# Kernel tuning notes

Measured on AMD Instinct MI355X. Metric: run time of the kernel, lower is better.

## Reference

```python
import jax, jax.numpy as jnp
import numpy as np

KD = 3  # kernel size per spatial dim
K = KD * KD * KD  # 27 taps


def conv3d(x, w, b, padding=1):
    # x: [B, C, D, H, W], w: [O, C, kd, kh, kw]
    pad = ((padding, padding),) * 3
    y = jax.lax.conv_general_dilated(
        x, w, window_strides=(1, 1, 1), padding=pad,
        dimension_numbers=('NCDHW', 'OIDHW', 'NCDHW'))
    return y + b[None, :, None, None, None]


def add_coords(x):
    # CoordConv: append 3 normalized coordinate channels in [-1, 1].
    B, C, D, H, W = x.shape
    z = jnp.linspace(-1.0, 1.0, D, dtype=x.dtype)[:, None, None]
    y = jnp.linspace(-1.0, 1.0, H, dtype=x.dtype)[None, :, None]
    xx = jnp.linspace(-1.0, 1.0, W, dtype=x.dtype)[None, None, :]
    coords = jnp.stack([
        jnp.broadcast_to(z, (D, H, W)),
        jnp.broadcast_to(y, (D, H, W)),
        jnp.broadcast_to(xx, (D, H, W)),
    ], axis=0)  # [3, D, H, W]
    coords = jnp.broadcast_to(coords[None], (B, 3, D, H, W))
    return jnp.concatenate([x, coords], axis=1)


def trilinear_sample(x, pos):
    # x: [B, C, D, H, W]; pos: [B, K, 3, D, H, W] absolute (z, y, x) sample coords.
    # Zero padding outside the volume. Returns [B, C, K, D, H, W].
    B, C, D, H, W = x.shape
    Kt = pos.shape[1]
    pz, py, px = pos[:, :, 0], pos[:, :, 1], pos[:, :, 2]  # [B, K, D, H, W]
    fz, fy, fx = jnp.floor(pz), jnp.floor(py), jnp.floor(px)
    x_flat = x.reshape(B, C, D * H * W)
    out = jnp.zeros((B, C, Kt, D, H, W), dtype=x.dtype)
    for cz in (0.0, 1.0):
        for cy in (0.0, 1.0):
            for cx in (0.0, 1.0):
                iz, iy, ix = fz + cz, fy + cy, fx + cx
                wgt = ((1.0 - jnp.abs(pz - iz)) *
                       (1.0 - jnp.abs(py - iy)) *
                       (1.0 - jnp.abs(px - ix)))
                valid = ((iz >= 0) & (iz < D) & (iy >= 0) & (iy < H)
                         & (ix >= 0) & (ix < W))
                izc = jnp.clip(iz, 0, D - 1).astype(jnp.int32)
                iyc = jnp.clip(iy, 0, H - 1).astype(jnp.int32)
                ixc = jnp.clip(ix, 0, W - 1).astype(jnp.int32)
                flat = ((izc * H + iyc) * W + ixc).reshape(B, -1)  # [B, K*DHW]
                vals = jax.vmap(lambda xf, idx: jnp.take(xf, idx, axis=1))(x_flat, flat)
                vals = vals.reshape(B, C, Kt, D, H, W)
                out = out + (wgt * valid.astype(x.dtype))[:, None] * vals
    return out


def modulated_deform_conv3d(x, offsets, alpha, w, b):
    # x: [B, Cin, D, H, W]; offsets: [B, 3K, D, H, W]; alpha: [B, K, D, H, W]
    # w: [O, Cin, 3, 3, 3]; stride 1, padding 1, dilation 1.
    B, Cin, D, H, W = x.shape
    off = offsets.reshape(B, K, 3, D, H, W)
    # Base sampling grid per tap: voxel position + kernel offset (pad=1 -> -1..1).
    dz = jnp.arange(D, dtype=x.dtype)[:, None, None]
    dy = jnp.arange(H, dtype=x.dtype)[None, :, None]
    dx = jnp.arange(W, dtype=x.dtype)[None, None, :]
    base = jnp.stack([
        jnp.broadcast_to(dz, (D, H, W)),
        jnp.broadcast_to(dy, (D, H, W)),
        jnp.broadcast_to(dx, (D, H, W)),
    ], axis=0)  # [3, D, H, W]
    kg = jnp.arange(KD, dtype=x.dtype) - 1.0  # [-1, 0, 1]
    kpos = jnp.stack(jnp.meshgrid(kg, kg, kg, indexing='ij'),
                     axis=-1).reshape(K, 3)  # [K, 3] in (kd, kh, kw) order
    pos = base[None, None] + kpos[None, :, :, None, None, None] + off  # [B,K,3,D,H,W]
    sampled = trilinear_sample(x, pos)  # [B, Cin, K, D, H, W]
    sampled = sampled * alpha[:, None]  # modulation
    wk = w.reshape(w.shape[0], Cin, K)
    out = jnp.einsum('bckv,ock->bov', sampled.reshape(B, Cin, K, D * H * W), wk)
    return out.reshape(B, -1, D, H, W) + b[None, :, None, None, None]


def setup_inputs() -> dict:
    key = jax.random.key(0)
    ks = jax.random.split(key, 4)
    B, Cin, Cout, D, H, W = 2, 64, 64, 8, 32, 32
    x = jax.random.normal(ks[0], (B, Cin, D, H, W), dtype=jnp.float32)
    # Small init on offset branch keeps sampling near the regular grid.
    w_off = jax.random.normal(ks[1], (108, Cin + 3, 3, 3, 3), jnp.float32) * 0.01
    b_off = jnp.zeros((108,), jnp.float32)
    w_dcn = jax.random.normal(ks[2], (Cout, Cin, 3, 3, 3), jnp.float32) * (1.0 / np.sqrt(Cin * 27))
    b_dcn = jnp.zeros((Cout,), jnp.float32)
    return {"x": x, "w_off": w_off, "b_off": b_off, "w_dcn": w_dcn, "b_dcn": b_dcn}


def reference(x, w_off, b_off, w_dcn, b_dcn):
    # CoordConv3d offset/mask prediction
    pred = conv3d(add_coords(x), w_off, b_off, padding=1)  # [B, 108, D, H, W]
    offsets, alpha = pred[:, :81], pred[:, 81:]
    alpha = jax.nn.sigmoid(alpha)  # [B, 27, D, H, W]
    return modulated_deform_conv3d(x, offsets, alpha, w_dcn, b_dcn)
```

## Files before the change

kernel.cpp:

```cpp
#include <hip/hip_runtime.h>

#define DHW  8192
#define COFF 108

typedef __attribute__((ext_vector_type(8))) short bf16x8;
typedef __attribute__((ext_vector_type(4))) float f32x4;
typedef __bf16 bfv2 __attribute__((ext_vector_type(2)));

__device__ inline unsigned short f2bf(float f) {
    unsigned u = __float_as_uint(f);
    u += 0x7fffu + ((u >> 16) & 1u);
    return (unsigned short)(u >> 16);
}
__device__ inline float bf2f(unsigned short h) {
    return __uint_as_float(((unsigned)h) << 16);
}

__device__ inline float dot2bf(unsigned a, unsigned b, float c) {
#if defined(__has_builtin) && __has_builtin(__builtin_amdgcn_fdot2_f32_bf16)
    return __builtin_amdgcn_fdot2_f32_bf16(__builtin_bit_cast(bfv2, a),
                                           __builtin_bit_cast(bfv2, b), c, false);
#else
    c += __uint_as_float(a << 16) * __uint_as_float(b << 16);
    c += __uint_as_float(a & 0xffff0000u) * __uint_as_float(b & 0xffff0000u);
    return c;
#endif
}

__global__ __launch_bounds__(256) void k_prep(
    const float* __restrict__ x, const float* __restrict__ w_off,
    const float* __restrict__ w_dcn,
    ushort* __restrict__ xt, ushort* __restrict__ pA1,
    ushort* __restrict__ pAc, ushort* __restrict__ pW)
{
    __shared__ ushort tile[16 * 66];
    const int bi = blockIdx.x;
    const int tid = threadIdx.x;
    if (bi < 1024) {
        const int b  = bi >> 9;
        const int f0 = (bi & 511) * 16;
        #pragma unroll
        for (int it = 0; it < 4; ++it) {
            int c = it * 16 + (tid >> 4), f = tid & 15;
            tile[f * 66 + c] = f2bf(x[((size_t)(b * 64 + c)) * DHW + f0 + f]);
        }
        __syncthreads();
        #pragma unroll
        for (int it = 0; it < 4; ++it) {
            int f = it * 4 + (tid >> 6), c = tid & 63;
            xt[((size_t)b * DHW + f0 + f) * 64 + c] = tile[f * 66 + c];
        }
    } else {
        int t0 = (bi - 1024) * 256 + tid;
        const int stride = 32 * 256;
        for (int i = t0; i < 27 * 2 * 7 * 512; i += stride) {
            int j = i & 7, l = (i >> 3) & 63, rest = i >> 9;
            int m = rest % 7, ch = (rest / 7) & 1, tap = rest / 14;
            int co = m * 16 + (l & 15);
            int ci = ch * 32 + (l >> 4) * 8 + j;
            pA1[i] = (co < COFF) ? f2bf(w_off[(co * 67 + ci) * 27 + tap]) : (ushort)0;
        }
        for (int i = t0; i < 3 * 7 * 512; i += stride) {
            int j = i & 7, l = (i >> 3) & 63, rest = i >> 9;
            int m = rest % 7, t = rest / 7;
            int co = m * 16 + (l & 15);
            int flatk = t * 32 + (l >> 4) * 8 + j;
            ushort v = 0;
            if (co < COFF && flatk < 81) {
                int cc = flatk / 27, tap = flatk % 27;
                v = f2bf(w_off[(co * 67 + 64 + cc) * 27 + tap]);
            }
            pAc[i] = v;
        }
        for (int i = t0; i < 27 * 2 * 4 * 512; i += stride) {
            int j = i & 7, l = (i >> 3) & 63;
            int m = (i >> 9) & 3, ch = (i >> 11) & 1, k = i >> 12;
            int o = m * 16 + (l & 15);
            int c = ch * 32 + (l >> 4) * 8 + j;
            pW[i] = f2bf(w_dcn[(o * 64 + c) * 27 + k]);
        }
    }
}

__global__ __launch_bounds__(512, 4) void k_fused(
    const ushort* __restrict__ xt, const ushort* __restrict__ pA1,
    const ushort* __restrict__ pAc, const ushort* __restrict__ pW,
    const float* __restrict__ b_off, const float* __restrict__ b_dcn,
    float* __restrict__ out)
{
    __shared__ __align__(16) char smem[64256];
    ushort* pred_lds = (ushort*)smem;
    char*   region   = smem + 6912;

    const int bi   = blockIdx.x;
    const int b    = bi >> 8;
    const int sp32 = bi & 255;
    const int d    = sp32 >> 5;
    const int h    = sp32 & 31;
    const int spg  = sp32 * 32;
    const int tid  = threadIdx.x;
    const int wv = tid >> 6, lane = tid & 63, q = lane >> 4, r16 = lane & 15;
    const ushort* __restrict__ xb = xt + (size_t)b * DHW * 64;

    f32x4 acc1[14] = {};
    for (int c = wv; c < 57; c += 8) {
        bf16x8 bf[2];
        const ushort* pa;
        if (c < 54) {
            int tap = c >> 1, ch = c & 1;
            int dz = tap / 9, rem9 = tap - dz * 9, dy = rem9 / 3, dx = rem9 - dy * 3;
            int zz = d + dz - 1, yy = h + dy - 1;
            int basepos = (zz << 10) + (yy << 5);
            bool okzy = ((unsigned)zz < 8u) & ((unsigned)yy < 32u);
            #pragma unroll
            for (int pt = 0; pt < 2; ++pt) {
                int xx = pt * 16 + r16 + dx - 1;
                bool ok = okzy & ((unsigned)xx < 32u);
                bf16x8 tv = {};
                if (ok) tv = *(const bf16x8*)(xb + (size_t)(basepos + xx) * 64
                                              + ch * 32 + q * 8);
                bf[pt] = tv;
            }
            pa = pA1 + (size_t)((tap * 2 + ch) * 7) * 512 + lane * 8;
        } else {
            int t = c - 54;
            #pragma unroll
            for (int pt = 0; pt < 2; ++pt) {
                bf16x8 bt;
                #pragma unroll
                for (int j = 0; j < 8; ++j) {
                    int flatk = t * 32 + q * 8 + j;
                    int cc = flatk / 27, tap = flatk % 27;
                    int dz = tap / 9, rem9 = tap - dz * 9, dy = rem9 / 3, dx = rem9 - dy * 3;
                    int zz = d + dz - 1, yy = h + dy - 1, xx = pt * 16 + r16 + dx - 1;
                    bool ok = (flatk < 81) & ((unsigned)zz < 8u) & ((unsigned)yy < 32u)
                              & ((unsigned)xx < 32u);
                    float val = 0.f;
                    if (ok)
                        val = (cc == 0) ? (-1.f + (2.f / 7.f) * (float)zz)
                            : (cc == 1) ? (-1.f + (2.f / 31.f) * (float)yy)
                                        : (-1.f + (2.f / 31.f) * (float)xx);
                    bt[j] = (short)f2bf(val);
                }
                bf[pt] = bt;
            }
            pa = pAc + (size_t)(t * 7) * 512 + lane * 8;
        }
        #pragma unroll
        for (int m = 0; m < 7; ++m) {
            bf16x8 af = *(const bf16x8*)(pa + m * 512);
            acc1[m * 2 + 0] = __builtin_amdgcn_mfma_f32_16x16x32_bf16(af, bf[0], acc1[m * 2 + 0], 0, 0, 0);
            acc1[m * 2 + 1] = __builtin_amdgcn_mfma_f32_16x16x32_bf16(af, bf[1], acc1[m * 2 + 1], 0, 0, 0);
        }
    }
    {
        uint2* red1 = (uint2*)region;
        #pragma unroll
        for (int i = 0; i < 14; ++i) {
            f32x4 s = acc1[i];
            uint2 pk2;
            pk2.x = (unsigned)f2bf(s[0]) | ((unsigned)f2bf(s[1]) << 16);
            pk2.y = (unsigned)f2bf(s[2]) | ((unsigned)f2bf(s[3]) << 16);
            red1[(wv * 14 + i) * 64 + lane] = pk2;
        }
        __syncthreads();
        for (int i = wv; i < 14; i += 8) {
            float s0 = 0.f, s1 = 0.f, s2 = 0.f, s3 = 0.f;
            #pragma unroll
            for (int sw = 0; sw < 8; ++sw) {
                uint2 v = red1[(sw * 14 + i) * 64 + lane];
                s0 += bf2f((unsigned short)(v.x & 0xffffu));
                s1 += bf2f((unsigned short)(v.x >> 16));
                s2 += bf2f((unsigned short)(v.y & 0xffffu));
                s3 += bf2f((unsigned short)(v.y >> 16));
            }
            int m = i >> 1, pt = i & 1;
            float sr[4] = {s0, s1, s2, s3};
            #pragma unroll
            for (int r = 0; r < 4; ++r) {
                int co = m * 16 + q * 4 + r;
                if (co < COFF)
                    pred_lds[co * 32 + pt * 16 + r16] = f2bf(sr[r] + b_off[co]);
            }
        }
        __syncthreads();
    }

    uint4* cwi = (uint4*)region;
    uint4* cww = (uint4*)(region + 27648);
    for (int kp = tid; kp < 27 * 32; kp += 512) {
        int k = kp >> 5, p = kp & 31;
        float offz = bf2f(pred_lds[(k * 3 + 0) * 32 + p]);
        float offy = bf2f(pred_lds[(k * 3 + 1) * 32 + p]);
        float offx = bf2f(pred_lds[(k * 3 + 2) * 32 + p]);
        float av   = bf2f(pred_lds[(81 + k) * 32 + p]);
        float alpha = 1.f / (1.f + __expf(-av));
        int kz = k / 9, rem = k - kz * 9, ky = rem / 3, kx = rem - ky * 3;
        float pz = (float)(d + kz - 1) + offz;
        float py = (float)(h + ky - 1) + offy;
        float px = (float)(p + kx - 1) + offx;
        float fz = floorf(pz), fy = floorf(py), fx = floorf(px);
        float tz = pz - fz, ty = py - fy, tx = px - fx;
        int iz0 = (int)fz, iy0 = (int)fy, ix0 = (int)fx;
        unsigned idxs[8]; float wgts[8];
        #pragma unroll
        for (int c8 = 0; c8 < 8; ++c8) {
            int czi = c8 >> 2, cyi = (c8 >> 1) & 1, cxi = c8 & 1;
            int iz = iz0 + czi, iy = iy0 + cyi, ix = ix0 + cxi;
            float wz = czi ? tz : 1.f - tz;
            float wy = cyi ? ty : 1.f - ty;
            float wx = cxi ? tx : 1.f - tx;
            bool ok = ((unsigned)iz < 8u) && ((unsigned)iy < 32u) && ((unsigned)ix < 32u);
            idxs[c8] = ok ? ((unsigned)((iz << 10) + (iy << 5) + ix) << 7) : 0u;
            wgts[c8] = ok ? wz * wy * wx * alpha : 0.f;
        }
        cwi[(k * 2 + 0) * 32 + p] = make_uint4(idxs[0], idxs[1], idxs[2], idxs[3]);
        cwi[(k * 2 + 1) * 32 + p] = make_uint4(idxs[4], idxs[5], idxs[6], idxs[7]);
        cww[k * 32 + p] = make_uint4(
            (unsigned)f2bf(wgts[0]) | ((unsigned)f2bf(wgts[1]) << 16),
            (unsigned)f2bf(wgts[2]) | ((unsigned)f2bf(wgts[3]) << 16),
            (unsigned)f2bf(wgts[4]) | ((unsigned)f2bf(wgts[5]) << 16),
            (unsigned)f2bf(wgts[6]) | ((unsigned)f2bf(wgts[7]) << 16));
    }
    __syncthreads();

    const int pt2 = wv & 1, ch2 = (wv >> 1) & 1, kh = wv >> 2;
    const int pr = lane >> 2, cg = lane & 3;
    const int p2 = pt2 * 16 + pr;
    const char* xbB = (const char*)xb + ch2 * 64 + cg * 16;
    const int baddr = (r16 * 4 + q) << 2;
    f32x4 acc2[4] = {};
    for (int k = kh; k < 27; k += 2) {
        uint4 wq = cww[k * 32 + p2];
        uint4 i0 = cwi[(k * 2 + 0) * 32 + p2];
        uint4 i1 = cwi[(k * 2 + 1) * 32 + p2];
        unsigned iv[8] = {i0.x, i0.y, i0.z, i0.w, i1.x, i1.y, i1.z, i1.w};
        uint4 xv[8];
        #pragma unroll
        for (int c8 = 0; c8 < 8; ++c8)
            xv[c8] = *(const uint4*)(xbB + iv[c8]);
        unsigned wp[4] = {wq.x, wq.y, wq.z, wq.w};
        float sa[8] = {};
        #pragma unroll
        for (int cp = 0; cp < 4; ++cp) {
            unsigned ua[4] = {xv[cp * 2 + 0].x, xv[cp * 2 + 0].y, xv[cp * 2 + 0].z, xv[cp * 2 + 0].w};
            unsigned ub[4] = {xv[cp * 2 + 1].x, xv[cp * 2 + 1].y, xv[cp * 2 + 1].z, xv[cp * 2 + 1].w};
            #pragma unroll
            for (int dw = 0; dw < 4; ++dw) {
                unsigned plo = __builtin_amdgcn_perm(ub[dw], ua[dw], 0x05040100u);
                unsigned phi = __builtin_amdgcn_perm(ub[dw], ua[dw], 0x07060302u);
                sa[dw * 2 + 0] = dot2bf(plo, wp[cp], sa[dw * 2 + 0]);
                sa[dw * 2 + 1] = dot2bf(phi, wp[cp], sa[dw * 2 + 1]);
            }
        }
        unsigned pk0 = (unsigned)f2bf(sa[0]) | ((unsigned)f2bf(sa[1]) << 16);
        unsigned pk1 = (unsigned)f2bf(sa[2]) | ((unsigned)f2bf(sa[3]) << 16);
        unsigned pk2 = (unsigned)f2bf(sa[4]) | ((unsigned)f2bf(sa[5]) << 16);
        unsigned pk3 = (unsigned)f2bf(sa[6]) | ((unsigned)f2bf(sa[7]) << 16);
        uint4 bd;
        bd.x = (unsigned)__builtin_amdgcn_ds_bpermute(baddr, (int)pk0);
        bd.y = (unsigned)__builtin_amdgcn_ds_bpermute(baddr, (int)pk1);
        bd.z = (unsigned)__builtin_amdgcn_ds_bpermute(baddr, (int)pk2);
        bd.w = (unsigned)__builtin_amdgcn_ds_bpermute(baddr, (int)pk3);
        bf16x8 bfrag = __builtin_bit_cast(bf16x8, bd);
        const ushort* pwk = pW + (size_t)((k * 2 + ch2) * 4) * 512 + lane * 8;
        #pragma unroll
        for (int m = 0; m < 4; ++m)
            acc2[m] = __builtin_amdgcn_mfma_f32_16x16x32_bf16(
                *(const bf16x8*)(pwk + m * 512), bfrag, acc2[m], 0, 0, 0);
    }

    __syncthreads();
    f32x4* red2 = (f32x4*)region;
    #pragma unroll
    for (int m = 0; m < 4; ++m)
        red2[(wv * 4 + m) * 64 + lane] = acc2[m];
    __syncthreads();
    {
        const int mo = wv >> 1, pto = wv & 1;
        f32x4 s = red2[((pto + 0) * 4 + mo) * 64 + lane]
                + red2[((pto + 2) * 4 + mo) * 64 + lane]
                + red2[((pto + 4) * 4 + mo) * 64 + lane]
                + red2[((pto + 6) * 4 + mo) * 64 + lane];
        float* __restrict__ outb = out + (size_t)b * 64 * DHW + spg;
        #pragma unroll
        for (int r = 0; r < 4; ++r) {
            int o = mo * 16 + q * 4 + r;
            outb[(size_t)o * DHW + pto * 16 + r16] = s[r] + b_dcn[o];
        }
    }
}

extern "C" void kernel_launch(void* const* d_in, const int* in_sizes, int n_in,
                              void* d_out, int out_size, void* d_ws, size_t ws_size,
                              hipStream_t stream) {
    const float* x     = (const float*)d_in[0];
    const float* w_off = (const float*)d_in[1];
    const float* b_off = (const float*)d_in[2];
    const float* w_dcn = (const float*)d_in[3];
    const float* b_dcn = (const float*)d_in[4];
    float* out = (float*)d_out;

    ushort* xt  = (ushort*)d_ws;
    ushort* pA1 = (ushort*)((char*)d_ws + 2097152);
    ushort* pAc = (ushort*)((char*)d_ws + 2484224);
    ushort* pW  = (ushort*)((char*)d_ws + 2505728);

    k_prep <<<1056, 256, 0, stream>>>(x, w_off, w_dcn, xt, pA1, pAc, pW);
    k_fused<<<512, 512, 0, stream>>>(xt, pA1, pAc, pW, b_off, b_dcn, out);
}
```

Before: 64.42 us.

## Split fused kernel into offset-conv and deform-conv kernels with double-buffered gathers

The single fused kernel is split in two. The first computes the offset/mask convolution and writes the prediction to a global workspace buffer in bf16. The second reads that buffer, builds the sampling indices and weights, and runs the deformable gather+MFMA loop with software double-buffering, so the gathers for tap k+2 are issued before the compute for tap k. The goal is to give each kernel lower LDS and register pressure and to hide gather latency, at the cost of an extra launch and a global round trip for the predictions.

Measured after the change: 68.60 us. 6.5% more time.

```diff
diff --git a/kernel.cpp b/kernel.cpp
--- a/kernel.cpp
+++ b/kernel.cpp
@@ -82,15 +82,12 @@
     }
 }
 
-__global__ __launch_bounds__(512, 4) void k_fused(
+__global__ __launch_bounds__(512, 4) void k_conv(
     const ushort* __restrict__ xt, const ushort* __restrict__ pA1,
-    const ushort* __restrict__ pAc, const ushort* __restrict__ pW,
-    const float* __restrict__ b_off, const float* __restrict__ b_dcn,
-    float* __restrict__ out)
+    const ushort* __restrict__ pAc, const float* __restrict__ b_off,
+    ushort* __restrict__ predg)
 {
-    __shared__ __align__(16) char smem[64256];
-    ushort* pred_lds = (ushort*)smem;
-    char*   region   = smem + 6912;
+    __shared__ __align__(16) char smem[57344];
 
     const int bi   = blockIdx.x;
     const int b    = bi >> 8;
@@ -153,47 +150,110 @@
             acc1[m * 2 + 1] = __builtin_amdgcn_mfma_f32_16x16x32_bf16(af, bf[1], acc1[m * 2 + 1], 0, 0, 0);
         }
     }
-    {
-        uint2* red1 = (uint2*)region;
-        #pragma unroll
-        for (int i = 0; i < 14; ++i) {
-            f32x4 s = acc1[i];
-            uint2 pk2;
-            pk2.x = (unsigned)f2bf(s[0]) | ((unsigned)f2bf(s[1]) << 16);
-            pk2.y = (unsigned)f2bf(s[2]) | ((unsigned)f2bf(s[3]) << 16);
-            red1[(wv * 14 + i) * 64 + lane] = pk2;
-        }
-        __syncthreads();
-        for (int i = wv; i < 14; i += 8) {
-            float s0 = 0.f, s1 = 0.f, s2 = 0.f, s3 = 0.f;
-            #pragma unroll
-            for (int sw = 0; sw < 8; ++sw) {
-                uint2 v = red1[(sw * 14 + i) * 64 + lane];
-                s0 += bf2f((unsigned short)(v.x & 0xffffu));
-                s1 += bf2f((unsigned short)(v.x >> 16));
-                s2 += bf2f((unsigned short)(v.y & 0xffffu));
-                s3 += bf2f((unsigned short)(v.y >> 16));
-            }
-            int m = i >> 1, pt = i & 1;
-            float sr[4] = {s0, s1, s2, s3};
-            #pragma unroll
-            for (int r = 0; r < 4; ++r) {
-                int co = m * 16 + q * 4 + r;
-                if (co < COFF)
-                    pred_lds[co * 32 + pt * 16 + r16] = f2bf(sr[r] + b_off[co]);
-            }
-        }
-        __syncthreads();
-    }
-
-    uint4* cwi = (uint4*)region;
-    uint4* cww = (uint4*)(region + 27648);
+    uint2* red1 = (uint2*)smem;
+    #pragma unroll
+    for (int i = 0; i < 14; ++i) {
+        f32x4 s = acc1[i];
+        uint2 pk2;
+        pk2.x = (unsigned)f2bf(s[0]) | ((unsigned)f2bf(s[1]) << 16);
+        pk2.y = (unsigned)f2bf(s[2]) | ((unsigned)f2bf(s[3]) << 16);
+        red1[(wv * 14 + i) * 64 + lane] = pk2;
+    }
+    __syncthreads();
+    ushort* __restrict__ predb = predg + (size_t)b * COFF * DHW + spg;
+    for (int i = wv; i < 14; i += 8) {
+        float s0 = 0.f, s1 = 0.f, s2 = 0.f, s3 = 0.f;
+        #pragma unroll
+        for (int sw = 0; sw < 8; ++sw) {
+            uint2 v = red1[(sw * 14 + i) * 64 + lane];
+            s0 += bf2f((unsigned short)(v.x & 0xffffu));
+            s1 += bf2f((unsigned short)(v.x >> 16));
+            s2 += bf2f((unsigned short)(v.y & 0xffffu));
+            s3 += bf2f((unsigned short)(v.y >> 16));
+        }
+        int m = i >> 1, pt = i & 1;
+        float sr[4] = {s0, s1, s2, s3};
+        #pragma unroll
+        for (int r = 0; r < 4; ++r) {
+            int co = m * 16 + q * 4 + r;
+            if (co < COFF)
+                predb[(size_t)co * DHW + pt * 16 + r16] = f2bf(sr[r] + b_off[co]);
+        }
+    }
+}
+
+#define LOADCW(X, kk) do {                                                    \
+    uint4 wq_ = cww[(kk) * 32 + p2];                                          \
+    uint4 i0_ = cwi[((kk) * 2 + 0) * 32 + p2];                                \
+    uint4 i1_ = cwi[((kk) * 2 + 1) * 32 + p2];                                \
+    wp##X[0] = wq_.x; wp##X[1] = wq_.y; wp##X[2] = wq_.z; wp##X[3] = wq_.w;   \
+    xv##X[0] = *(const uint4*)(xbB + i0_.x);                                  \
+    xv##X[1] = *(const uint4*)(xbB + i0_.y);                                  \
+    xv##X[2] = *(const uint4*)(xbB + i0_.z);                                  \
+    xv##X[3] = *(const uint4*)(xbB + i0_.w);                                  \
+    xv##X[4] = *(const uint4*)(xbB + i1_.x);                                  \
+    xv##X[5] = *(const uint4*)(xbB + i1_.y);                                  \
+    xv##X[6] = *(const uint4*)(xbB + i1_.z);                                  \
+    xv##X[7] = *(const uint4*)(xbB + i1_.w);                                  \
+} while (0)
+
+#define COMPUTE(X, kk) do {                                                   \
+    float sa[8] = {0.f, 0.f, 0.f, 0.f, 0.f, 0.f, 0.f, 0.f};                   \
+    _Pragma("unroll")                                                         \
+    for (int cp = 0; cp < 4; ++cp) {                                          \
+        unsigned ua[4] = {xv##X[cp*2].x, xv##X[cp*2].y, xv##X[cp*2].z, xv##X[cp*2].w};       \
+        unsigned ub[4] = {xv##X[cp*2+1].x, xv##X[cp*2+1].y, xv##X[cp*2+1].z, xv##X[cp*2+1].w};\
+        _Pragma("unroll")                                                     \
+        for (int dw = 0; dw < 4; ++dw) {                                      \
+            unsigned plo = __builtin_amdgcn_perm(ub[dw], ua[dw], 0x05040100u);\
+            unsigned phi = __builtin_amdgcn_perm(ub[dw], ua[dw], 0x07060302u);\
+            sa[dw * 2 + 0] = dot2bf(plo, wp##X[cp], sa[dw * 2 + 0]);          \
+            sa[dw * 2 + 1] = dot2bf(phi, wp##X[cp], sa[dw * 2 + 1]);          \
+        }                                                                     \
+    }                                                                         \
+    unsigned pk0 = (unsigned)f2bf(sa[0]) | ((unsigned)f2bf(sa[1]) << 16);     \
+    unsigned pk1 = (unsigned)f2bf(sa[2]) | ((unsigned)f2bf(sa[3]) << 16);     \
+    unsigned pk2_ = (unsigned)f2bf(sa[4]) | ((unsigned)f2bf(sa[5]) << 16);    \
+    unsigned pk3 = (unsigned)f2bf(sa[6]) | ((unsigned)f2bf(sa[7]) << 16);     \
+    uint4 bd;                                                                 \
+    bd.x = (unsigned)__builtin_amdgcn_ds_bpermute(baddr, (int)pk0);           \
+    bd.y = (unsigned)__builtin_amdgcn_ds_bpermute(baddr, (int)pk1);           \
+    bd.z = (unsigned)__builtin_amdgcn_ds_bpermute(baddr, (int)pk2_);          \
+    bd.w = (unsigned)__builtin_amdgcn_ds_bpermute(baddr, (int)pk3);           \
+    bf16x8 bfrag = __builtin_bit_cast(bf16x8, bd);                            \
+    const ushort* pwk = pW + (size_t)(((kk) * 2 + ch2) * 4) * 512 + lane * 8; \
+    _Pragma("unroll")                                                         \
+    for (int m = 0; m < 4; ++m)                                               \
+        acc2[m] = __builtin_amdgcn_mfma_f32_16x16x32_bf16(                    \
+            *(const bf16x8*)(pwk + m * 512), bfrag, acc2[m], 0, 0, 0);        \
+} while (0)
+
+__global__ __launch_bounds__(512, 4) void k_dcn2(
+    const ushort* __restrict__ xt, const ushort* __restrict__ predg,
+    const ushort* __restrict__ pW, const float* __restrict__ b_dcn,
+    float* __restrict__ out)
+{
+    __shared__ __align__(16) char smem[41472];
+
+    const int bi   = blockIdx.x;
+    const int b    = bi >> 8;
+    const int sp32 = bi & 255;
+    const int d    = sp32 >> 5;
+    const int h    = sp32 & 31;
+    const int spg  = sp32 * 32;
+    const int tid  = threadIdx.x;
+    const int wv = tid >> 6, lane = tid & 63, q = lane >> 4, r16 = lane & 15;
+    const ushort* __restrict__ xb = xt + (size_t)b * DHW * 64;
+    const ushort* __restrict__ predb = predg + (size_t)b * COFF * DHW + spg;
+
+    uint4* cwi = (uint4*)smem;
+    uint4* cww = (uint4*)(smem + 27648);
     for (int kp = tid; kp < 27 * 32; kp += 512) {
         int k = kp >> 5, p = kp & 31;
-        float offz = bf2f(pred_lds[(k * 3 + 0) * 32 + p]);
-        float offy = bf2f(pred_lds[(k * 3 + 1) * 32 + p]);
-        float offx = bf2f(pred_lds[(k * 3 + 2) * 32 + p]);
-        float av   = bf2f(pred_lds[(81 + k) * 32 + p]);
+        float offz = bf2f(predb[(k * 3 + 0) * DHW + p]);
+        float offy = bf2f(predb[(k * 3 + 1) * DHW + p]);
+        float offx = bf2f(predb[(k * 3 + 2) * DHW + p]);
+        float av   = bf2f(predb[(81 + k) * DHW + p]);
         float alpha = 1.f / (1.f + __expf(-av));
         int kz = k / 9, rem = k - kz * 9, ky = rem / 3, kx = rem - ky * 3;
         float pz = (float)(d + kz - 1) + offz;
@@ -230,48 +290,24 @@
     const char* xbB = (const char*)xb + ch2 * 64 + cg * 16;
     const int baddr = (r16 * 4 + q) << 2;
     f32x4 acc2[4] = {};
-    for (int k = kh; k < 27; k += 2) {
-        uint4 wq = cww[k * 32 + p2];
-        uint4 i0 = cwi[(k * 2 + 0) * 32 + p2];
-        uint4 i1 = cwi[(k * 2 + 1) * 32 + p2];
-        unsigned iv[8] = {i0.x, i0.y, i0.z, i0.w, i1.x, i1.y, i1.z, i1.w};
-        uint4 xv[8];
-        #pragma unroll
-        for (int c8 = 0; c8 < 8; ++c8)
-            xv[c8] = *(const uint4*)(xbB + iv[c8]);
-        unsigned wp[4] = {wq.x, wq.y, wq.z, wq.w};
-        float sa[8] = {};
-        #pragma unroll
-        for (int cp = 0; cp < 4; ++cp) {
-            unsigned ua[4] = {xv[cp * 2 + 0].x, xv[cp * 2 + 0].y, xv[cp * 2 + 0].z, xv[cp * 2 + 0].w};
-            unsigned ub[4] = {xv[cp * 2 + 1].x, xv[cp * 2 + 1].y, xv[cp * 2 + 1].z, xv[cp * 2 + 1].w};
-            #pragma unroll
-            for (int dw = 0; dw < 4; ++dw) {
-                unsigned plo = __builtin_amdgcn_perm(ub[dw], ua[dw], 0x05040100u);
-                unsigned phi = __builtin_amdgcn_perm(ub[dw], ua[dw], 0x07060302u);
-                sa[dw * 2 + 0] = dot2bf(plo, wp[cp], sa[dw * 2 + 0]);
-                sa[dw * 2 + 1] = dot2bf(phi, wp[cp], sa[dw * 2 + 1]);
-            }
-        }
-        unsigned pk0 = (unsigned)f2bf(sa[0]) | ((unsigned)f2bf(sa[1]) << 16);
-        unsigned pk1 = (unsigned)f2bf(sa[2]) | ((unsigned)f2bf(sa[3]) << 16);
-        unsigned pk2 = (unsigned)f2bf(sa[4]) | ((unsigned)f2bf(sa[5]) << 16);
-        unsigned pk3 = (unsigned)f2bf(sa[6]) | ((unsigned)f2bf(sa[7]) << 16);
-        uint4 bd;
-        bd.x = (unsigned)__builtin_amdgcn_ds_bpermute(baddr, (int)pk0);
-        bd.y = (unsigned)__builtin_amdgcn_ds_bpermute(baddr, (int)pk1);
-        bd.z = (unsigned)__builtin_amdgcn_ds_bpermute(baddr, (int)pk2);
-        bd.w = (unsigned)__builtin_amdgcn_ds_bpermute(baddr, (int)pk3);
-        bf16x8 bfrag = __builtin_bit_cast(bf16x8, bd);
-        const ushort* pwk = pW + (size_t)((k * 2 + ch2) * 4) * 512 + lane * 8;
-        #pragma unroll
-        for (int m = 0; m < 4; ++m)
-            acc2[m] = __builtin_amdgcn_mfma_f32_16x16x32_bf16(
-                *(const bf16x8*)(pwk + m * 512), bfrag, acc2[m], 0, 0, 0);
+
+    uint4 xvA[8], xvB[8];
+    unsigned wpA[4], wpB[4];
+    int k = kh;
+    LOADCW(A, k);
+    while (true) {
+        if (k + 2 < 27) LOADCW(B, k + 2);
+        COMPUTE(A, k);
+        k += 2;
+        if (k >= 27) break;
+        if (k + 2 < 27) LOADCW(A, k + 2);
+        COMPUTE(B, k);
+        k += 2;
+        if (k >= 27) break;
     }
 
     __syncthreads();
-    f32x4* red2 = (f32x4*)region;
+    f32x4* red2 = (f32x4*)smem;
     #pragma unroll
     for (int m = 0; m < 4; ++m)
         red2[(wv * 4 + m) * 64 + lane] = acc2[m];
@@ -301,11 +337,13 @@
     const float* b_dcn = (const float*)d_in[4];
     float* out = (float*)d_out;
 
-    ushort* xt  = (ushort*)d_ws;
-    ushort* pA1 = (ushort*)((char*)d_ws + 2097152);
-    ushort* pAc = (ushort*)((char*)d_ws + 2484224);
-    ushort* pW  = (ushort*)((char*)d_ws + 2505728);
-
-    k_prep <<<1056, 256, 0, stream>>>(x, w_off, w_dcn, xt, pA1, pAc, pW);
-    k_fused<<<512, 512, 0, stream>>>(xt, pA1, pAc, pW, b_off, b_dcn, out);
-}
+    ushort* xt   = (ushort*)d_ws;
+    ushort* pA1  = (ushort*)((char*)d_ws + 2097152);
+    ushort* pAc  = (ushort*)((char*)d_ws + 2484224);
+    ushort* pW   = (ushort*)((char*)d_ws + 2505728);
+    ushort* pred = (ushort*)((char*)d_ws + 2726912);
+
+    k_prep<<<1056, 256, 0, stream>>>(x, w_off, w_dcn, xt, pA1, pAc, pW);
+    k_conv<<<512, 512, 0, stream>>>(xt, pA1, pAc, b_off, pred);
+    k_dcn2<<<512, 512, 0, stream>>>(xt, pred, pW, b_dcn, out);
+}
```

## Split fused kernel into conv and deform kernels with LDS halo slab

Applied to the files above, without the earlier changes.

Splits the fused kernel into two. The first runs the offset convolution and writes the bf16 prediction to global workspace. The second kernel, over 2048 smaller blocks that each handle 16 voxels and one channel half, stages a 5x5x20 halo slab of x in swizzled LDS and gathers bilinear taps from it, falling back to global loads only when a tap falls outside the window. The two channel halves are combined with atomicAdd into an output zeroed by a memset first. This trades an extra launch, a global round-trip of the prediction and atomics for better gather locality and more parallelism.

Result: slower. 82.52 us (+28.1%).

```diff
diff --git a/kernel.cpp b/kernel.cpp
--- a/kernel.cpp
+++ b/kernel.cpp
@@ -82,15 +82,12 @@
     }
 }
 
-__global__ __launch_bounds__(512, 4) void k_fused(
+__global__ __launch_bounds__(512, 4) void k_conv(
     const ushort* __restrict__ xt, const ushort* __restrict__ pA1,
-    const ushort* __restrict__ pAc, const ushort* __restrict__ pW,
-    const float* __restrict__ b_off, const float* __restrict__ b_dcn,
-    float* __restrict__ out)
+    const ushort* __restrict__ pAc, const float* __restrict__ b_off,
+    ushort* __restrict__ predg)
 {
-    __shared__ __align__(16) char smem[64256];
-    ushort* pred_lds = (ushort*)smem;
-    char*   region   = smem + 6912;
+    __shared__ __align__(16) char smem[57344];
 
     const int bi   = blockIdx.x;
     const int b    = bi >> 8;
@@ -153,56 +150,89 @@
             acc1[m * 2 + 1] = __builtin_amdgcn_mfma_f32_16x16x32_bf16(af, bf[1], acc1[m * 2 + 1], 0, 0, 0);
         }
     }
-    {
-        uint2* red1 = (uint2*)region;
-        #pragma unroll
-        for (int i = 0; i < 14; ++i) {
-            f32x4 s = acc1[i];
-            uint2 pk2;
-            pk2.x = (unsigned)f2bf(s[0]) | ((unsigned)f2bf(s[1]) << 16);
-            pk2.y = (unsigned)f2bf(s[2]) | ((unsigned)f2bf(s[3]) << 16);
-            red1[(wv * 14 + i) * 64 + lane] = pk2;
-        }
-        __syncthreads();
-        for (int i = wv; i < 14; i += 8) {
-            float s0 = 0.f, s1 = 0.f, s2 = 0.f, s3 = 0.f;
-            #pragma unroll
-            for (int sw = 0; sw < 8; ++sw) {
-                uint2 v = red1[(sw * 14 + i) * 64 + lane];
-                s0 += bf2f((unsigned short)(v.x & 0xffffu));
-                s1 += bf2f((unsigned short)(v.x >> 16));
-                s2 += bf2f((unsigned short)(v.y & 0xffffu));
-                s3 += bf2f((unsigned short)(v.y >> 16));
-            }
-            int m = i >> 1, pt = i & 1;
-            float sr[4] = {s0, s1, s2, s3};
-            #pragma unroll
-            for (int r = 0; r < 4; ++r) {
-                int co = m * 16 + q * 4 + r;
-                if (co < COFF)
-                    pred_lds[co * 32 + pt * 16 + r16] = f2bf(sr[r] + b_off[co]);
-            }
-        }
-        __syncthreads();
-    }
-
-    uint4* cwi = (uint4*)region;
-    uint4* cww = (uint4*)(region + 27648);
-    for (int kp = tid; kp < 27 * 32; kp += 512) {
-        int k = kp >> 5, p = kp & 31;
-        float offz = bf2f(pred_lds[(k * 3 + 0) * 32 + p]);
-        float offy = bf2f(pred_lds[(k * 3 + 1) * 32 + p]);
-        float offx = bf2f(pred_lds[(k * 3 + 2) * 32 + p]);
-        float av   = bf2f(pred_lds[(81 + k) * 32 + p]);
+    uint2* red1 = (uint2*)smem;
+    #pragma unroll
+    for (int i = 0; i < 14; ++i) {
+        f32x4 s = acc1[i];
+        uint2 pk2;
+        pk2.x = (unsigned)f2bf(s[0]) | ((unsigned)f2bf(s[1]) << 16);
+        pk2.y = (unsigned)f2bf(s[2]) | ((unsigned)f2bf(s[3]) << 16);
+        red1[(wv * 14 + i) * 64 + lane] = pk2;
+    }
+    __syncthreads();
+    ushort* __restrict__ predb = predg + (size_t)b * COFF * DHW + spg;
+    for (int i = wv; i < 14; i += 8) {
+        float s0 = 0.f, s1 = 0.f, s2 = 0.f, s3 = 0.f;
+        #pragma unroll
+        for (int sw = 0; sw < 8; ++sw) {
+            uint2 v = red1[(sw * 14 + i) * 64 + lane];
+            s0 += bf2f((unsigned short)(v.x & 0xffffu));
+            s1 += bf2f((unsigned short)(v.x >> 16));
+            s2 += bf2f((unsigned short)(v.y & 0xffffu));
+            s3 += bf2f((unsigned short)(v.y >> 16));
+        }
+        int m = i >> 1, pt = i & 1;
+        float sr[4] = {s0, s1, s2, s3};
+        #pragma unroll
+        for (int r = 0; r < 4; ++r) {
+            int co = m * 16 + q * 4 + r;
+            if (co < COFF)
+                predb[(size_t)co * DHW + pt * 16 + r16] = f2bf(sr[r] + b_off[co]);
+        }
+    }
+}
+
+__global__ __launch_bounds__(256, 3) void k_dcn3(
+    const ushort* __restrict__ xt, const ushort* __restrict__ predg,
+    const ushort* __restrict__ pW, const float* __restrict__ b_dcn,
+    float* __restrict__ out)
+{
+    __shared__ __align__(16) char smem[53184];
+    char*  slab = smem;
+    uint4* cwi  = (uint4*)(smem + 32000);
+    uint4* cww  = (uint4*)(smem + 45824);
+    unsigned char* tagb = (unsigned char*)(smem + 52736);
+
+    const int bi   = blockIdx.x;
+    const int ch2  = bi & 1;
+    const int sp16 = (bi >> 1) & 511;
+    const int b    = bi >> 10;
+    const int d    = sp16 >> 6;
+    const int h    = (sp16 >> 1) & 31;
+    const int x0   = (sp16 & 1) * 16;
+    const int spg  = sp16 * 16;
+    const int tid  = threadIdx.x;
+    const int wv = tid >> 6, lane = tid & 63, q = lane >> 4, r16 = lane & 15;
+    const ushort* __restrict__ xb = xt + (size_t)b * DHW * 64;
+    const ushort* __restrict__ predb = predg + (size_t)b * COFF * DHW + spg;
+
+    for (int idx = tid; idx < 2000; idx += 256) {
+        int pos = idx >> 2, slot = idx & 3;
+        int sz = pos / 100, rem = pos - sz * 100, sy = rem / 20, sx = rem - sy * 20;
+        int gz = d - 2 + sz, gy = h - 2 + sy, gx = x0 - 2 + sx;
+        uint4 v = {};
+        if (((unsigned)gz < 8u) && ((unsigned)gy < 32u) && ((unsigned)gx < 32u))
+            v = *(const uint4*)(xb + (size_t)((gz << 10) + (gy << 5) + gx) * 64
+                                + ch2 * 32 + slot * 8);
+        *(uint4*)(slab + pos * 64 + ((slot ^ (pos & 3)) << 4)) = v;
+    }
+
+    for (int kp = tid; kp < 432; kp += 256) {
+        int k = kp >> 4, p = kp & 15;
+        float offz = bf2f(predb[(k * 3 + 0) * DHW + p]);
+        float offy = bf2f(predb[(k * 3 + 1) * DHW + p]);
+        float offx = bf2f(predb[(k * 3 + 2) * DHW + p]);
+        float av   = bf2f(predb[(81 + k) * DHW + p]);
         float alpha = 1.f / (1.f + __expf(-av));
         int kz = k / 9, rem = k - kz * 9, ky = rem / 3, kx = rem - ky * 3;
         float pz = (float)(d + kz - 1) + offz;
         float py = (float)(h + ky - 1) + offy;
-        float px = (float)(p + kx - 1) + offx;
+        float px = (float)(x0 + p + kx - 1) + offx;
         float fz = floorf(pz), fy = floorf(py), fx = floorf(px);
         float tz = pz - fz, ty = py - fy, tx = px - fx;
         int iz0 = (int)fz, iy0 = (int)fy, ix0 = (int)fx;
-        unsigned idxs[8]; float wgts[8];
+        unsigned glob[8], linb[8]; float wgts[8];
+        bool anyoow = false;
         #pragma unroll
         for (int c8 = 0; c8 < 8; ++c8) {
             int czi = c8 >> 2, cyi = (c8 >> 1) & 1, cxi = c8 & 1;
@@ -211,34 +241,62 @@
             float wy = cyi ? ty : 1.f - ty;
             float wx = cxi ? tx : 1.f - tx;
             bool ok = ((unsigned)iz < 8u) && ((unsigned)iy < 32u) && ((unsigned)ix < 32u);
-            idxs[c8] = ok ? ((unsigned)((iz << 10) + (iy << 5) + ix) << 7) : 0u;
+            int szw = iz - d + 2, syw = iy - h + 2, sxw = ix - x0 + 2;
+            bool inw = ((unsigned)szw < 5u) && ((unsigned)syw < 5u) && ((unsigned)sxw < 20u);
+            if (ok && !inw) anyoow = true;
             wgts[c8] = ok ? wz * wy * wx * alpha : 0.f;
-        }
-        cwi[(k * 2 + 0) * 32 + p] = make_uint4(idxs[0], idxs[1], idxs[2], idxs[3]);
-        cwi[(k * 2 + 1) * 32 + p] = make_uint4(idxs[4], idxs[5], idxs[6], idxs[7]);
-        cww[k * 32 + p] = make_uint4(
+            glob[c8] = ok ? ((unsigned)((iz << 10) + (iy << 5) + ix) << 7) : 0u;
+            int szc = szw < 0 ? 0 : (szw > 4 ? 4 : szw);
+            int syc = syw < 0 ? 0 : (syw > 4 ? 4 : syw);
+            int sxc = sxw < 0 ? 0 : (sxw > 19 ? 19 : sxw);
+            linb[c8] = (unsigned)(((szc * 5 + syc) * 20 + sxc) << 6);
+        }
+        uint4 w0_, w1_;
+        if (anyoow) {
+            w0_ = make_uint4(glob[0], glob[1], glob[2], glob[3]);
+            w1_ = make_uint4(glob[4], glob[5], glob[6], glob[7]);
+        } else {
+            w0_ = make_uint4(linb[0], linb[1], linb[2], linb[3]);
+            w1_ = make_uint4(linb[4], linb[5], linb[6], linb[7]);
+        }
+        cwi[(k * 2 + 0) * 16 + p] = w0_;
+        cwi[(k * 2 + 1) * 16 + p] = w1_;
+        cww[k * 16 + p] = make_uint4(
             (unsigned)f2bf(wgts[0]) | ((unsigned)f2bf(wgts[1]) << 16),
             (unsigned)f2bf(wgts[2]) | ((unsigned)f2bf(wgts[3]) << 16),
             (unsigned)f2bf(wgts[4]) | ((unsigned)f2bf(wgts[5]) << 16),
             (unsigned)f2bf(wgts[6]) | ((unsigned)f2bf(wgts[7]) << 16));
+        tagb[kp] = anyoow ? 1 : 0;
     }
     __syncthreads();
 
-    const int pt2 = wv & 1, ch2 = (wv >> 1) & 1, kh = wv >> 2;
     const int pr = lane >> 2, cg = lane & 3;
-    const int p2 = pt2 * 16 + pr;
-    const char* xbB = (const char*)xb + ch2 * 64 + cg * 16;
+    const char* __restrict__ xbG = (const char*)xb + ch2 * 64 + cg * 16;
     const int baddr = (r16 * 4 + q) << 2;
+    const unsigned cgsh = (unsigned)(cg << 4);
     f32x4 acc2[4] = {};
-    for (int k = kh; k < 27; k += 2) {
-        uint4 wq = cww[k * 32 + p2];
-        uint4 i0 = cwi[(k * 2 + 0) * 32 + p2];
-        uint4 i1 = cwi[(k * 2 + 1) * 32 + p2];
+    const int kbeg = wv * 7;
+    const int kend = (kbeg + 7 < 27) ? (kbeg + 7) : 27;
+    for (int k = kbeg; k < kend; ++k) {
+        uint4 wq = cww[k * 16 + pr];
+        uint4 i0 = cwi[(k * 2 + 0) * 16 + pr];
+        uint4 i1 = cwi[(k * 2 + 1) * 16 + pr];
         unsigned iv[8] = {i0.x, i0.y, i0.z, i0.w, i1.x, i1.y, i1.z, i1.w};
+        bool tg = tagb[k * 16 + pr] != 0;
         uint4 xv[8];
-        #pragma unroll
-        for (int c8 = 0; c8 < 8; ++c8)
-            xv[c8] = *(const uint4*)(xbB + iv[c8]);
+        if (!tg) {
+            #pragma unroll
+            for (int c8 = 0; c8 < 8; ++c8) {
+                unsigned a = iv[c8];
+                unsigned addr = a + (cgsh ^ ((a >> 2) & 0x30u));
+                xv[c8] = *(const uint4*)(slab + addr);
+            }
+        }
+        if (tg) {
+            #pragma unroll
+            for (int c8 = 0; c8 < 8; ++c8)
+                xv[c8] = *(const uint4*)(xbG + iv[c8]);
+        }
         unsigned wp[4] = {wq.x, wq.y, wq.z, wq.w};
         float sa[8] = {};
         #pragma unroll
@@ -271,22 +329,23 @@
     }
 
     __syncthreads();
-    f32x4* red2 = (f32x4*)region;
+    f32x4* red2 = (f32x4*)(smem + 32000);
     #pragma unroll
     for (int m = 0; m < 4; ++m)
         red2[(wv * 4 + m) * 64 + lane] = acc2[m];
     __syncthreads();
     {
-        const int mo = wv >> 1, pto = wv & 1;
-        f32x4 s = red2[((pto + 0) * 4 + mo) * 64 + lane]
-                + red2[((pto + 2) * 4 + mo) * 64 + lane]
-                + red2[((pto + 4) * 4 + mo) * 64 + lane]
-                + red2[((pto + 6) * 4 + mo) * 64 + lane];
+        const int mo = wv;
+        f32x4 s = red2[(0 * 4 + mo) * 64 + lane]
+                + red2[(1 * 4 + mo) * 64 + lane]
+                + red2[(2 * 4 + mo) * 64 + lane]
+                + red2[(3 * 4 + mo) * 64 + lane];
         float* __restrict__ outb = out + (size_t)b * 64 * DHW + spg;
         #pragma unroll
         for (int r = 0; r < 4; ++r) {
             int o = mo * 16 + q * 4 + r;
-            outb[(size_t)o * DHW + pto * 16 + r16] = s[r] + b_dcn[o];
+            float v = s[r] + (ch2 == 0 ? b_dcn[o] : 0.f);
+            atomicAdd(&outb[(size_t)o * DHW + r16], v);
         }
     }
 }
@@ -301,11 +360,14 @@
     const float* b_dcn = (const float*)d_in[4];
     float* out = (float*)d_out;
 
-    ushort* xt  = (ushort*)d_ws;
-    ushort* pA1 = (ushort*)((char*)d_ws + 2097152);
-    ushort* pAc = (ushort*)((char*)d_ws + 2484224);
-    ushort* pW  = (ushort*)((char*)d_ws + 2505728);
-
-    k_prep <<<1056, 256, 0, stream>>>(x, w_off, w_dcn, xt, pA1, pAc, pW);
-    k_fused<<<512, 512, 0, stream>>>(xt, pA1, pAc, pW, b_off, b_dcn, out);
-}
+    ushort* xt   = (ushort*)d_ws;
+    ushort* pA1  = (ushort*)((char*)d_ws + 2097152);
+    ushort* pAc  = (ushort*)((char*)d_ws + 2484224);
+    ushort* pW   = (ushort*)((char*)d_ws + 2505728);
+    ushort* pred = (ushort*)((char*)d_ws + 2726912);
+
+    hipMemsetAsync(out, 0, (size_t)out_size * sizeof(float), stream);
+    k_prep<<<1056, 256, 0, stream>>>(x, w_off, w_dcn, xt, pA1, pAc, pW);
+    k_conv<<<512, 512, 0, stream>>>(xt, pA1, pAc, b_off, pred);
+    k_dcn3<<<2048, 256, 0, stream>>>(xt, pred, pW, b_dcn, out);
+}
```
